# Kernel optimization log

Measured on AMD Instinct MI355X. Metric: run time of the kernel, lower is better.

## Reference

```python
import jax, jax.numpy as jnp
import numpy as np

DIM = 256
HEADS = 8
DIM_HEAD = 64
INNER = HEADS * DIM_HEAD  # 512
SCALE = DIM_HEAD ** -0.5
EPS = 1e-5


def _layernorm(x, w, b):
    mu = jnp.mean(x, axis=-1, keepdims=True)
    var = jnp.var(x, axis=-1, keepdims=True)
    return (x - mu) * jax.lax.rsqrt(var + EPS) * w + b


def setup_inputs() -> dict:
    key = jax.random.key(0)
    ks = jax.random.split(key, 20)
    B, N, M, H, W = 8, 4096, 256, 64, 64
    s = 0.02
    inp = {
        "feat": jax.random.normal(ks[0], (B, N, DIM), jnp.float32),
        "center": jax.random.normal(ks[1], (B, M, DIM), jnp.float32),
        "pos": jax.random.normal(ks[2], (B, DIM, H, W), jnp.float32),
        "center_pos": jax.random.normal(ks[3], (B, M, DIM), jnp.float32),
        # projection weights stored [in, out] so y = x @ W
        "Wq": jax.random.normal(ks[4], (DIM, INNER), jnp.float32) * s,
        "Wk": jax.random.normal(ks[5], (DIM, INNER), jnp.float32) * s,
        "Wv1": jax.random.normal(ks[6], (DIM, INNER), jnp.float32) * s,
        "Wv2": jax.random.normal(ks[7], (DIM, INNER), jnp.float32) * s,
        "Wo1": jax.random.normal(ks[8], (INNER, DIM), jnp.float32) * s,
        "Wo2": jax.random.normal(ks[9], (INNER, DIM), jnp.float32) * s,
        "ln1_w": jnp.ones((DIM,), jnp.float32),
        "ln1_b": jnp.zeros((DIM,), jnp.float32),
        "ln2_w": jnp.ones((DIM,), jnp.float32),
        "ln2_b": jnp.zeros((DIM,), jnp.float32),
        "ffn1_W1": jax.random.normal(ks[10], (DIM, DIM), jnp.float32) * s,
        "ffn1_W2": jax.random.normal(ks[11], (DIM, DIM), jnp.float32) * s,
        "ffn1_b2": jnp.zeros((DIM,), jnp.float32),
        "ffn2_W1": jax.random.normal(ks[12], (DIM, DIM), jnp.float32) * s,
        "ffn2_W2": jax.random.normal(ks[13], (DIM, DIM), jnp.float32) * s,
        "ffn2_b2": jnp.zeros((DIM,), jnp.float32),
    }
    return inp


def reference(feat, center, pos, center_pos, Wq, Wk, Wv1, Wv2, Wo1, Wo2,
              ln1_w, ln1_b, ln2_w, ln2_b, ffn1_W1, ffn1_W2, ffn1_b2,
              ffn2_W1, ffn2_W2, ffn2_b2):
    B = feat.shape[0]
    # pos: [B, C, H, W] -> [B, N, C]
    pos_f = pos.reshape(B, DIM, -1).transpose(0, 2, 1)
    q = (feat + pos_f) @ Wq            # [B, N, INNER]
    k = (center + center_pos) @ Wk     # [B, M, INNER]
    v1 = feat @ Wv1                    # [B, N, INNER]
    v2 = center @ Wv2                  # [B, M, INNER]

    def split(x):  # [B, T, h*d] -> [B, h, T, d]
        return x.reshape(B, x.shape[1], HEADS, DIM_HEAD).transpose(0, 2, 1, 3)

    q, k, v1, v2 = split(q), split(k), split(v1), split(v2)
    attn = jnp.einsum("bhnd,bhmd->bhnm", q, k) * SCALE  # [B, h, N, M]
    attn1 = jax.nn.softmax(attn, axis=-2)  # over N (queries)
    attn2 = jax.nn.softmax(attn, axis=-1)  # over M (keys)
    out_feat = jnp.einsum("bhnm,bhmd->bhnd", attn2, v2)    # [B, h, N, d]
    out_center = jnp.einsum("bhnm,bhnd->bhmd", attn1, v1)  # [B, h, M, d]

    def merge(x):  # [B, h, T, d] -> [B, T, h*d]
        return x.transpose(0, 2, 1, 3).reshape(B, x.shape[2], INNER)

    out_feat = merge(out_feat) @ Wo1 + feat
    out_center = merge(out_center) @ Wo2 + center
    out_feat = _layernorm(out_feat, ln1_w, ln1_b)
    out_center = _layernorm(out_center, ln2_w, ln2_b)
    out_feat = jax.nn.relu(out_feat @ ffn1_W1) @ ffn1_W2 + ffn1_b2 + out_feat
    out_center = jax.nn.relu(out_center @ ffn2_W1) @ ffn2_W2 + ffn2_b2 + out_center
    return out_feat, out_center
```

## Files before the change

kernel.cpp:

```cpp
#include <hip/hip_runtime.h>

typedef __bf16 bf16;
typedef __bf16 bf16x4 __attribute__((ext_vector_type(4)));
typedef __bf16 bf16x8 __attribute__((ext_vector_type(8)));
typedef float f32x4 __attribute__((ext_vector_type(4)));

#define MFMA16(a, b, c) __builtin_amdgcn_mfma_f32_16x16x32_bf16(a, b, c, 0, 0, 0)

#define CEXP 0.18033688011112042f

struct WTArgs {
  const float* src[10];
  bf16* dst[10];
  int K[10];
  int N[10];
};

__global__ __launch_bounds__(256) void wtrans_kernel(WTArgs args) {
  const int z = blockIdx.z;
  const int K = args.K[z], N = args.N[z];
  const int k0 = blockIdx.x * 64, n0 = blockIdx.y * 64;
  if (k0 >= K || n0 >= N) return;
  __shared__ float t[64][65];
  const int tx = threadIdx.x & 63, ty = threadIdx.x >> 6;
  const float* __restrict__ src = args.src[z];
  bf16* __restrict__ dst = args.dst[z];
#pragma unroll
  for (int i = 0; i < 16; ++i)
    t[ty + i * 4][tx] = src[(size_t)(k0 + ty + i * 4) * N + n0 + tx];
  __syncthreads();
#pragma unroll
  for (int i = 0; i < 16; ++i)
    dst[(size_t)(n0 + ty + i * 4) * K + k0 + tx] = (bf16)t[tx][ty + i * 4];
}

__global__ __launch_bounds__(256) void prep_xq_kernel(
    const float* __restrict__ feat, const float* __restrict__ pos,
    bf16* __restrict__ xq) {
  const int n0 = blockIdx.x * 64;
  const int c0 = blockIdx.y * 64;
  const int b = blockIdx.z;
  __shared__ float t[64][65];
  const int tx = threadIdx.x & 63, ty = threadIdx.x >> 6;
#pragma unroll
  for (int i = 0; i < 16; ++i) {
    int c = ty + i * 4;
    t[c][tx] = pos[((size_t)b * 256 + c0 + c) * 4096 + n0 + tx];
  }
  __syncthreads();
#pragma unroll
  for (int i = 0; i < 16; ++i) {
    int n = ty + i * 4;
    size_t off = ((size_t)b * 4096 + n0 + n) * 256 + c0 + tx;
    xq[off] = (bf16)(feat[off] + t[tx][n]);
  }
}

__global__ __launch_bounds__(256) void addvec_kernel(
    const float* __restrict__ a, const float* __restrict__ b,
    bf16* __restrict__ o, int n4) {
  int i = blockIdx.x * 256 + threadIdx.x;
  if (i < n4) {
    f32x4 x = ((const f32x4*)a)[i];
    f32x4 y = ((const f32x4*)b)[i];
    bf16x4 z;
#pragma unroll
    for (int j = 0; j < 4; ++j) z[j] = (bf16)(x[j] + y[j]);
    ((bf16x4*)o)[i] = z;
  }
}

__device__ inline void stage16(const bf16* g, bf16* l) {
  __builtin_amdgcn_global_load_lds(
      (const __attribute__((address_space(1))) void*)g,
      (__attribute__((address_space(3))) void*)l, 16, 0, 0);
}
__device__ inline void stage16(const float* g, bf16* l) {
  f32x4 u = *(const f32x4*)g;
  f32x4 v = *((const f32x4*)g + 1);
  bf16x8 o;
#pragma unroll
  for (int i = 0; i < 4; ++i) {
    o[i] = (bf16)u[i];
    o[4 + i] = (bf16)v[i];
  }
  *(bf16x8*)l = o;
}

template <int EPI, typename TO, typename TR, typename TA>
__global__ __launch_bounds__(256) void gemm_kernel(
    const TA* __restrict__ A, const bf16* __restrict__ BT,
    TO* __restrict__ C, const TR* __restrict__ resid,
    const float* __restrict__ bias, int M, int N, int K) {
  const int m0 = blockIdx.x * 128;
  const int n0 = blockIdx.y * 128;
  const int tid = threadIdx.x;
  const int lane = tid & 63;
  const int w = tid >> 6;
  const int wr = (w >> 1) * 64, wc = (w & 1) * 64;
  const int l15 = lane & 15, quad = lane >> 4;

  __shared__ __align__(16) bf16 Al[128 * 32];
  __shared__ __align__(16) bf16 Bl[128 * 32];

  f32x4 acc[4][4];
#pragma unroll
  for (int i = 0; i < 4; ++i)
#pragma unroll
    for (int j = 0; j < 4; ++j) acc[i][j] = (f32x4){0.f, 0.f, 0.f, 0.f};

  const int sw = (((l15 >> 1) & 3) ^ quad) * 8;

  for (int k0 = 0; k0 < K; k0 += 32) {
#pragma unroll
    for (int c = 0; c < 2; ++c) {
      int idx = tid + c * 256;
      int row = idx >> 2;
      int gs = ((idx & 3) ^ ((row >> 1) & 3)) * 8;
      stage16(A + (size_t)(m0 + row) * K + k0 + gs, Al + idx * 8);
      stage16(BT + (size_t)(n0 + row) * K + k0 + gs, Bl + idx * 8);
    }
    __syncthreads();
    bf16x8 fa[4], fb[4];
#pragma unroll
    for (int i = 0; i < 4; ++i) {
      fa[i] = *(const bf16x8*)(Al + (wr + i * 16 + l15) * 32 + sw);
      fb[i] = *(const bf16x8*)(Bl + (wc + i * 16 + l15) * 32 + sw);
    }
#pragma unroll
    for (int i = 0; i < 4; ++i)
#pragma unroll
      for (int j = 0; j < 4; ++j)
        acc[i][j] = MFMA16(fa[i], fb[j], acc[i][j]);
    __syncthreads();
  }

#pragma unroll
  for (int i = 0; i < 4; ++i) {
#pragma unroll
    for (int r = 0; r < 4; ++r) {
      int row = m0 + wr + i * 16 + quad * 4 + r;
      size_t rb = (size_t)row * N + n0 + wc;
#pragma unroll
      for (int j = 0; j < 4; ++j) {
        int col = j * 16 + l15;
        float v = acc[i][j][r];
        if constexpr (EPI == 1) v = fmaxf(v, 0.f);
        if constexpr (EPI == 2) v += (float)resid[rb + col];
        if constexpr (EPI == 3)
          v += bias[n0 + wc + col] + (float)resid[rb + col];
        C[rb + col] = (TO)v;
      }
    }
  }
}

__global__ __launch_bounds__(256, 1) void attf_kernel(
    const bf16* q, const bf16* __restrict__ kk, const bf16* __restrict__ v1,
    const bf16* __restrict__ v2, bf16* af, float* __restrict__ acc_p,
    float* __restrict__ colsum_p) {
  const int nb = blockIdx.x;
  const int h = blockIdx.y;
  const int b = blockIdx.z;
  const int tid = threadIdx.x;
  const int lane = tid & 63;
  const int w = tid >> 6;
  const int l15 = lane & 15, quad = lane >> 4;

  __shared__ __align__(16) bf16 klds[256 * 72];
  __shared__ __align__(16) bf16 v2T[64 * 264];
  __shared__ __align__(16) bf16 v1T[2][64 * 72];
  __shared__ __align__(16) bf16 PT[256 * 72];
  __shared__ __align__(16) bf16 Pl[4][16 * 264];

#pragma unroll
  for (int c = 0; c < 8; ++c) {
    int idx = tid + c * 256;
    int m = idx >> 3;
    int dc = (idx & 7) * 8;
    *(bf16x8*)(klds + m * 72 + dc) =
        *(const bf16x8*)(kk + ((size_t)(b * 256 + m)) * 512 + h * 64 + dc);
  }
#pragma unroll
  for (int c = 0; c < 8; ++c) {
    int idx = tid + c * 256;
    int m = idx >> 3;
    int dc = (idx & 7) * 8;
    bf16x8 t =
        *(const bf16x8*)(v2 + ((size_t)(b * 256 + m)) * 512 + h * 64 + dc);
#pragma unroll
    for (int j = 0; j < 8; ++j) v2T[(dc + j) * 264 + m] = t[j];
  }
  {
    const int nl = tid >> 3;
    const int dc = (tid & 7) * 8;
    const bf16* v1b =
        v1 + ((size_t)(b * 4096 + nb * 1024)) * 512 + h * 64 + dc;
    bf16x8 t0 = *(const bf16x8*)(v1b + (size_t)nl * 512);
    bf16x8 t1 = *(const bf16x8*)(v1b + (size_t)(nl + 32) * 512);
#pragma unroll
    for (int j = 0; j < 8; ++j) {
      v1T[0][(dc + j) * 72 + nl] = t0[j];
      v1T[0][(dc + j) * 72 + nl + 32] = t1[j];
    }
  }
  bf16x8 qa0, qa1;
  {
    int nrow = b * 4096 + nb * 1024 + w * 16 + l15;
    const bf16* qp = q + (size_t)nrow * 512 + h * 64 + quad * 8;
    qa0 = *(const bf16x8*)(qp);
    qa1 = *(const bf16x8*)(qp + 32);
  }

  f32x4 oc2[16];
#pragma unroll
  for (int i = 0; i < 16; ++i) oc2[i] = (f32x4){0.f, 0.f, 0.f, 0.f};
  float cs[16];
#pragma unroll
  for (int i = 0; i < 16; ++i) cs[i] = 0.f;

  __syncthreads();

#pragma unroll 2
  for (int ch = 0; ch < 16; ++ch) {
    bf16x8 v1a, v1b;
    const int nl = tid >> 3;
    const int dc = (tid & 7) * 8;
    if (ch < 15) {
      const bf16* v1p =
          v1 + ((size_t)(b * 4096 + nb * 1024 + (ch + 1) * 64)) * 512 +
          h * 64 + dc;
      v1a = *(const bf16x8*)(v1p + (size_t)nl * 512);
      v1b = *(const bf16x8*)(v1p + (size_t)(nl + 32) * 512);
    }

    float rs[4] = {0.f, 0.f, 0.f, 0.f};
#pragma unroll
    for (int mt = 0; mt < 16; ++mt) {
      const bf16* kp = klds + (mt * 16 + l15) * 72 + quad * 8;
      bf16x8 b0 = *(const bf16x8*)(kp);
      bf16x8 b1 = *(const bf16x8*)(kp + 32);
      f32x4 s = (f32x4){0.f, 0.f, 0.f, 0.f};
      s = MFMA16(qa0, b0, s);
      s = MFMA16(qa1, b1, s);
      float e0 = exp2f(s[0] * CEXP);
      float e1 = exp2f(s[1] * CEXP);
      float e2 = exp2f(s[2] * CEXP);
      float e3 = exp2f(s[3] * CEXP);
      rs[0] += e0; rs[1] += e1; rs[2] += e2; rs[3] += e3;
      cs[mt] += e0 + e1 + e2 + e3;
      Pl[w][(quad * 4 + 0) * 264 + mt * 16 + l15] = (bf16)e0;
      Pl[w][(quad * 4 + 1) * 264 + mt * 16 + l15] = (bf16)e1;
      Pl[w][(quad * 4 + 2) * 264 + mt * 16 + l15] = (bf16)e2;
      Pl[w][(quad * 4 + 3) * 264 + mt * 16 + l15] = (bf16)e3;
      bf16x4 ev;
      ev[0] = (bf16)e0; ev[1] = (bf16)e1; ev[2] = (bf16)e2; ev[3] = (bf16)e3;
      *(bf16x4*)(PT + (mt * 16 + l15) * 72 + w * 16 + quad * 4) = ev;
    }
    if (ch < 15) {
      bf16* dst = v1T[(ch + 1) & 1];
#pragma unroll
      for (int j = 0; j < 8; ++j) {
        dst[(dc + j) * 72 + nl] = v1a[j];
        dst[(dc + j) * 72 + nl + 32] = v1b[j];
      }
    }
    __syncthreads();

    bf16x8 qn0 = qa0, qn1 = qa1;
    if (ch < 15) {
      int nrow = b * 4096 + nb * 1024 + (ch + 1) * 64 + w * 16 + l15;
      const bf16* qp = q + (size_t)nrow * 512 + h * 64 + quad * 8;
      qn0 = *(const bf16x8*)(qp);
      qn1 = *(const bf16x8*)(qp + 32);
    }

    f32x4 o1[4];
#pragma unroll
    for (int i = 0; i < 4; ++i) o1[i] = (f32x4){0.f, 0.f, 0.f, 0.f};
#pragma unroll
    for (int ks = 0; ks < 8; ++ks) {
      bf16x8 pa = *(const bf16x8*)(Pl[w] + l15 * 264 + ks * 32 + quad * 8);
#pragma unroll
      for (int dt = 0; dt < 4; ++dt) {
        bf16x8 vb = *(const bf16x8*)(v2T + (dt * 16 + l15) * 264 + ks * 32 +
                                     quad * 8);
        o1[dt] = MFMA16(pa, vb, o1[dt]);
      }
    }
    float inv[4];
#pragma unroll
    for (int r = 0; r < 4; ++r) {
      float v = rs[r];
      v += __shfl_xor(v, 1, 64);
      v += __shfl_xor(v, 2, 64);
      v += __shfl_xor(v, 4, 64);
      v += __shfl_xor(v, 8, 64);
      inv[r] = 1.f / v;
    }
#pragma unroll
    for (int dt = 0; dt < 4; ++dt) {
#pragma unroll
      for (int r = 0; r < 4; ++r) {
        int n = nb * 1024 + ch * 64 + w * 16 + quad * 4 + r;
        af[((size_t)(b * 4096 + n)) * 512 + h * 64 + dt * 16 + l15] =
            (bf16)(o1[dt][r] * inv[r]);
      }
    }

    const bf16* vc = v1T[ch & 1];
#pragma unroll
    for (int ks = 0; ks < 2; ++ks) {
      bf16x8 vbv[4];
#pragma unroll
      for (int dt = 0; dt < 4; ++dt)
        vbv[dt] = *(const bf16x8*)(vc + (dt * 16 + l15) * 72 + ks * 32 +
                                   quad * 8);
#pragma unroll
      for (int mq = 0; mq < 4; ++mq) {
        bf16x8 pa2 = *(const bf16x8*)(PT + (mq * 64 + w * 16 + l15) * 72 +
                                      ks * 32 + quad * 8);
#pragma unroll
        for (int dt = 0; dt < 4; ++dt)
          oc2[mq * 4 + dt] = MFMA16(pa2, vbv[dt], oc2[mq * 4 + dt]);
      }
    }
    __syncthreads();
    qa0 = qn0;
    qa1 = qn1;
  }

  float* cw = (float*)klds;
#pragma unroll
  for (int t = 0; t < 16; ++t) {
    float v = cs[t];
    v += __shfl_xor(v, 16, 64);
    v += __shfl_xor(v, 32, 64);
    if (quad == 0) cw[w * 256 + t * 16 + l15] = v;
  }
  __syncthreads();
  {
    int m = tid;
    float s = cw[m] + cw[256 + m] + cw[512 + m] + cw[768 + m];
    colsum_p[((size_t)(nb * 64 + b * 8 + h)) * 256 + m] = s;
  }
  float* base = acc_p + ((size_t)(nb * 64 + b * 8 + h)) * 256 * 64;
#pragma unroll
  for (int mq = 0; mq < 4; ++mq) {
#pragma unroll
    for (int dt = 0; dt < 4; ++dt) {
#pragma unroll
      for (int r = 0; r < 4; ++r) {
        int m = mq * 64 + w * 16 + quad * 4 + r;
        base[m * 64 + dt * 16 + l15] = oc2[mq * 4 + dt][r];
      }
    }
  }
}

__global__ __launch_bounds__(256) void acm_kernel(
    const float* __restrict__ acc_p, const float* __restrict__ colsum_p,
    bf16* __restrict__ acm) {
  int idx = blockIdx.x * 256 + threadIdx.x;
  int d = idx & 63;
  int h = (idx >> 6) & 7;
  int m = (idx >> 9) & 255;
  int b = idx >> 17;
  float cv = 0.f, v = 0.f;
#pragma unroll
  for (int p = 0; p < 4; ++p) {
    cv += colsum_p[((size_t)(p * 64 + b * 8 + h)) * 256 + m];
    v += acc_p[(((size_t)(p * 64 + b * 8 + h)) * 256 + m) * 64 + d];
  }
  acm[idx] = (bf16)(v / cv);
}

__global__ __launch_bounds__(256) void ln_kernel(
    const bf16* __restrict__ x, const float* __restrict__ wv,
    const float* __restrict__ bv, bf16* __restrict__ y, int rows) {
  int wave = threadIdx.x >> 6;
  int lane = threadIdx.x & 63;
  int row = blockIdx.x * 4 + wave;
  if (row >= rows) return;
  const bf16* xr = x + (size_t)row * 256;
  bf16x4 v = *(const bf16x4*)(xr + lane * 4);
  float f0 = v[0], f1 = v[1], f2 = v[2], f3 = v[3];
  float s = f0 + f1 + f2 + f3;
  float ss = f0 * f0 + f1 * f1 + f2 * f2 + f3 * f3;
#pragma unroll
  for (int m = 1; m < 64; m <<= 1) {
    s += __shfl_xor(s, m, 64);
    ss += __shfl_xor(ss, m, 64);
  }
  float mean = s * (1.f / 256.f);
  float var = ss * (1.f / 256.f) - mean * mean;
  float rstd = rsqrtf(var + 1e-5f);
  f32x4 wq = *(const f32x4*)(wv + lane * 4);
  f32x4 bq = *(const f32x4*)(bv + lane * 4);
  bf16x4 o;
  o[0] = (bf16)((f0 - mean) * rstd * wq[0] + bq[0]);
  o[1] = (bf16)((f1 - mean) * rstd * wq[1] + bq[1]);
  o[2] = (bf16)((f2 - mean) * rstd * wq[2] + bq[2]);
  o[3] = (bf16)((f3 - mean) * rstd * wq[3] + bq[3]);
  *(bf16x4*)(y + (size_t)row * 256 + lane * 4) = o;
}

extern "C" void kernel_launch(void* const* d_in, const int* in_sizes, int n_in,
                              void* d_out, int out_size, void* d_ws,
                              size_t ws_size, hipStream_t stream) {
  const float* feat = (const float*)d_in[0];
  const float* center = (const float*)d_in[1];
  const float* pos = (const float*)d_in[2];
  const float* cpos = (const float*)d_in[3];
  const float* Wq = (const float*)d_in[4];
  const float* Wk = (const float*)d_in[5];
  const float* Wv1 = (const float*)d_in[6];
  const float* Wv2 = (const float*)d_in[7];
  const float* Wo1 = (const float*)d_in[8];
  const float* Wo2 = (const float*)d_in[9];
  const float* ln1w = (const float*)d_in[10];
  const float* ln1b = (const float*)d_in[11];
  const float* ln2w = (const float*)d_in[12];
  const float* ln2b = (const float*)d_in[13];
  const float* f1W1 = (const float*)d_in[14];
  const float* f1W2 = (const float*)d_in[15];
  const float* f1b2 = (const float*)d_in[16];
  const float* f2W1 = (const float*)d_in[17];
  const float* f2W2 = (const float*)d_in[18];
  const float* f2b2 = (const float*)d_in[19];

  char* ws = (char*)d_ws;
  const size_t MB = 1024 * 1024;
  bf16* q_ = (bf16*)(ws + 0);
  bf16* af_ = q_;
  bf16* v1_ = (bf16*)(ws + 32 * MB);
  bf16* xq_ = (bf16*)(ws + 64 * MB);
  float* accp_ = (float*)(ws + 64 * MB);
  bf16* rf_ = xq_;
  bf16* k_ = (bf16*)(ws + 80 * MB);
  bf16* xk_ = (bf16*)(ws + 82 * MB);
  bf16* rc_ = xk_;
  bf16* v2_ = (bf16*)(ws + 83 * MB);
  bf16* acm_ = v2_;
  float* colsum_ = (float*)(ws + 89 * MB);
  bf16* wt_ = (bf16*)(ws + 89 * MB + 262144);
  bf16* yf_ = q_;
  bf16* tf_ = (bf16*)(ws + 16 * MB);
  bf16* yc_ = (bf16*)(ws + 92 * MB);
  bf16* tc_ = (bf16*)(ws + 93 * MB);

  bf16* WqT = wt_;
  bf16* WkT = WqT + 131072;
  bf16* Wv1T = WkT + 131072;
  bf16* Wv2T = Wv1T + 131072;
  bf16* Wo1T = Wv2T + 131072;
  bf16* Wo2T = Wo1T + 131072;
  bf16* f1W1T = Wo2T + 131072;
  bf16* f1W2T = f1W1T + 65536;
  bf16* f2W1T = f1W2T + 65536;
  bf16* f2W2T = f2W1T + 65536;

  float* out_feat = (float*)d_out;
  float* out_center = out_feat + (size_t)8 * 4096 * 256;

  WTArgs wa;
  const float* srcs[10] = {Wq, Wk, Wv1, Wv2, Wo1, Wo2, f1W1, f1W2, f2W1, f2W2};
  bf16* dsts[10] = {WqT, WkT, Wv1T, Wv2T, Wo1T, Wo2T, f1W1T, f1W2T, f2W1T, f2W2T};
  int Ks[10] = {256, 256, 256, 256, 512, 512, 256, 256, 256, 256};
  int Ns[10] = {512, 512, 512, 512, 256, 256, 256, 256, 256, 256};
  for (int i = 0; i < 10; ++i) {
    wa.src[i] = srcs[i];
    wa.dst[i] = dsts[i];
    wa.K[i] = Ks[i];
    wa.N[i] = Ns[i];
  }

  wtrans_kernel<<<dim3(8, 8, 10), 256, 0, stream>>>(wa);
  prep_xq_kernel<<<dim3(64, 4, 8), 256, 0, stream>>>(feat, pos, xq_);
  addvec_kernel<<<dim3(512), 256, 0, stream>>>(center, cpos, xk_, 131072);

  gemm_kernel<0, bf16, bf16, bf16><<<dim3(256, 4), 256, 0, stream>>>(
      xq_, WqT, q_, nullptr, nullptr, 32768, 512, 256);
  gemm_kernel<0, bf16, bf16, bf16><<<dim3(16, 4), 256, 0, stream>>>(
      xk_, WkT, k_, nullptr, nullptr, 2048, 512, 256);
  gemm_kernel<0, bf16, bf16, float><<<dim3(256, 4), 256, 0, stream>>>(
      feat, Wv1T, v1_, nullptr, nullptr, 32768, 512, 256);
  gemm_kernel<0, bf16, bf16, float><<<dim3(16, 4), 256, 0, stream>>>(
      center, Wv2T, v2_, nullptr, nullptr, 2048, 512, 256);

  attf_kernel<<<dim3(4, 8, 8), 256, 0, stream>>>(q_, k_, v1_, v2_, af_, accp_,
                                                 colsum_);
  acm_kernel<<<dim3(4096), 256, 0, stream>>>(accp_, colsum_, acm_);

  gemm_kernel<2, bf16, float, bf16><<<dim3(256, 2), 256, 0, stream>>>(
      af_, Wo1T, rf_, feat, nullptr, 32768, 256, 512);
  ln_kernel<<<dim3(8192), 256, 0, stream>>>(rf_, ln1w, ln1b, yf_, 32768);
  gemm_kernel<1, bf16, bf16, bf16><<<dim3(256, 2), 256, 0, stream>>>(
      yf_, f1W1T, tf_, nullptr, nullptr, 32768, 256, 256);
  gemm_kernel<3, float, bf16, bf16><<<dim3(256, 2), 256, 0, stream>>>(
      tf_, f1W2T, out_feat, yf_, f1b2, 32768, 256, 256);

  gemm_kernel<2, bf16, float, bf16><<<dim3(16, 2), 256, 0, stream>>>(
      acm_, Wo2T, rc_, center, nullptr, 2048, 256, 512);
  ln_kernel<<<dim3(512), 256, 0, stream>>>(rc_, ln2w, ln2b, yc_, 2048);
  gemm_kernel<1, bf16, bf16, bf16><<<dim3(16, 2), 256, 0, stream>>>(
      yc_, f2W1T, tc_, nullptr, nullptr, 2048, 256, 256);
  gemm_kernel<3, float, bf16, bf16><<<dim3(16, 2), 256, 0, stream>>>(
      tc_, f2W2T, out_center, yc_, f2b2, 2048, 256, 256);
}
```

Before: 387.3 us.

## Batch feat/center GEMMs, fuse center add into K GEMM, vectorize epilogues

The center+center_pos add is folded into the K-projection GEMM's A staging, and paired feat/center GEMMs and layernorms now run as single launches using a blockIdx.z selector. MFMA operand order is swapped so each lane holds four consecutive columns. This lets the GEMM and attention epilogues write vectorized bf16x4/f32x4 stores instead of scattered scalar ones. The aim is fewer launches, less small-launch tail time, and better store coalescing. The cost is that the z=1 center launches spawn many blocks that return immediately.

```diff
diff --git a/kernel.cpp b/kernel.cpp
--- a/kernel.cpp
+++ b/kernel.cpp
@@ -56,20 +56,6 @@
   }
 }
 
-__global__ __launch_bounds__(256) void addvec_kernel(
-    const float* __restrict__ a, const float* __restrict__ b,
-    bf16* __restrict__ o, int n4) {
-  int i = blockIdx.x * 256 + threadIdx.x;
-  if (i < n4) {
-    f32x4 x = ((const f32x4*)a)[i];
-    f32x4 y = ((const f32x4*)b)[i];
-    bf16x4 z;
-#pragma unroll
-    for (int j = 0; j < 4; ++j) z[j] = (bf16)(x[j] + y[j]);
-    ((bf16x4*)o)[i] = z;
-  }
-}
-
 __device__ inline void stage16(const bf16* g, bf16* l) {
   __builtin_amdgcn_global_load_lds(
       (const __attribute__((address_space(1))) void*)g,
@@ -86,13 +72,52 @@
   }
   *(bf16x8*)l = o;
 }
-
-template <int EPI, typename TO, typename TR, typename TA>
-__global__ __launch_bounds__(256) void gemm_kernel(
-    const TA* __restrict__ A, const bf16* __restrict__ BT,
-    TO* __restrict__ C, const TR* __restrict__ resid,
-    const float* __restrict__ bias, int M, int N, int K) {
+__device__ inline void stage16(const float* g, const float* g2, bf16* l) {
+  f32x4 u = *(const f32x4*)g + *(const f32x4*)g2;
+  f32x4 v = *((const f32x4*)g + 1) + *((const f32x4*)g2 + 1);
+  bf16x8 o;
+#pragma unroll
+  for (int i = 0; i < 4; ++i) {
+    o[i] = (bf16)u[i];
+    o[4 + i] = (bf16)v[i];
+  }
+  *(bf16x8*)l = o;
+}
+
+__device__ inline f32x4 rload(const float* p) { return *(const f32x4*)p; }
+__device__ inline f32x4 rload(const bf16* p) {
+  bf16x4 t = *(const bf16x4*)p;
+  return (f32x4){(float)t[0], (float)t[1], (float)t[2], (float)t[3]};
+}
+__device__ inline void cstore(float* p, f32x4 v) { *(f32x4*)p = v; }
+__device__ inline void cstore(bf16* p, f32x4 v) {
+  bf16x4 o;
+  o[0] = (bf16)v[0]; o[1] = (bf16)v[1]; o[2] = (bf16)v[2]; o[3] = (bf16)v[3];
+  *(bf16x4*)p = o;
+}
+
+struct GArg {
+  const void* A[2];
+  const void* A2[2];
+  const bf16* BT[2];
+  void* C[2];
+  const void* resid[2];
+  const float* bias[2];
+  int M[2];
+};
+
+template <int EPI, typename TO, typename TR, typename TA, bool FUSE2>
+__global__ __launch_bounds__(256) void gemm_kernel(GArg g, int N, int K) {
+  const int z = blockIdx.z;
   const int m0 = blockIdx.x * 128;
+  if (m0 >= g.M[z]) return;
+  const TA* A = (const TA*)g.A[z];
+  const TA* A2 = (const TA*)g.A2[z];
+  const bf16* BT = g.BT[z];
+  TO* C = (TO*)g.C[z];
+  const TR* resid = (const TR*)g.resid[z];
+  const float* bias = g.bias[z];
+
   const int n0 = blockIdx.y * 128;
   const int tid = threadIdx.x;
   const int lane = tid & 63;
@@ -117,7 +142,11 @@
       int idx = tid + c * 256;
       int row = idx >> 2;
       int gs = ((idx & 3) ^ ((row >> 1) & 3)) * 8;
-      stage16(A + (size_t)(m0 + row) * K + k0 + gs, Al + idx * 8);
+      size_t aoff = (size_t)(m0 + row) * K + k0 + gs;
+      if constexpr (FUSE2)
+        stage16(A + aoff, A2 + aoff, Al + idx * 8);
+      else
+        stage16(A + aoff, Al + idx * 8);
       stage16(BT + (size_t)(n0 + row) * K + k0 + gs, Bl + idx * 8);
     }
     __syncthreads();
@@ -131,26 +160,26 @@
     for (int i = 0; i < 4; ++i)
 #pragma unroll
       for (int j = 0; j < 4; ++j)
-        acc[i][j] = MFMA16(fa[i], fb[j], acc[i][j]);
+        acc[i][j] = MFMA16(fb[j], fa[i], acc[i][j]);
     __syncthreads();
   }
 
 #pragma unroll
   for (int i = 0; i < 4; ++i) {
 #pragma unroll
-    for (int r = 0; r < 4; ++r) {
-      int row = m0 + wr + i * 16 + quad * 4 + r;
-      size_t rb = (size_t)row * N + n0 + wc;
-#pragma unroll
-      for (int j = 0; j < 4; ++j) {
-        int col = j * 16 + l15;
-        float v = acc[i][j][r];
-        if constexpr (EPI == 1) v = fmaxf(v, 0.f);
-        if constexpr (EPI == 2) v += (float)resid[rb + col];
-        if constexpr (EPI == 3)
-          v += bias[n0 + wc + col] + (float)resid[rb + col];
-        C[rb + col] = (TO)v;
+    for (int j = 0; j < 4; ++j) {
+      int row = m0 + wr + i * 16 + l15;
+      int col = n0 + wc + j * 16 + quad * 4;
+      size_t off = (size_t)row * N + col;
+      f32x4 v = acc[i][j];
+      if constexpr (EPI == 1) {
+#pragma unroll
+        for (int e = 0; e < 4; ++e) v[e] = fmaxf(v[e], 0.f);
       }
+      if constexpr (EPI == 2) v += rload(resid + off);
+      if constexpr (EPI == 3)
+        v += rload(resid + off) + *(const f32x4*)(bias + col);
+      cstore(C + off, v);
     }
   }
 }
@@ -285,10 +314,9 @@
       for (int dt = 0; dt < 4; ++dt) {
         bf16x8 vb = *(const bf16x8*)(v2T + (dt * 16 + l15) * 264 + ks * 32 +
                                      quad * 8);
-        o1[dt] = MFMA16(pa, vb, o1[dt]);
+        o1[dt] = MFMA16(vb, pa, o1[dt]);
       }
     }
-    float inv[4];
 #pragma unroll
     for (int r = 0; r < 4; ++r) {
       float v = rs[r];
@@ -296,15 +324,27 @@
       v += __shfl_xor(v, 2, 64);
       v += __shfl_xor(v, 4, 64);
       v += __shfl_xor(v, 8, 64);
-      inv[r] = 1.f / v;
-    }
-#pragma unroll
-    for (int dt = 0; dt < 4; ++dt) {
-#pragma unroll
-      for (int r = 0; r < 4; ++r) {
-        int n = nb * 1024 + ch * 64 + w * 16 + quad * 4 + r;
-        af[((size_t)(b * 4096 + n)) * 512 + h * 64 + dt * 16 + l15] =
-            (bf16)(o1[dt][r] * inv[r]);
+      rs[r] = v;
+    }
+    {
+      int srcq = (l15 >> 2) << 4;
+      float s0 = __shfl(rs[0], srcq, 64);
+      float s1 = __shfl(rs[1], srcq, 64);
+      float s2 = __shfl(rs[2], srcq, 64);
+      float s3 = __shfl(rs[3], srcq, 64);
+      float a01 = (l15 & 1) ? s1 : s0;
+      float a23 = (l15 & 1) ? s3 : s2;
+      float inv = 1.f / ((l15 & 2) ? a23 : a01);
+      int n = nb * 1024 + ch * 64 + w * 16 + l15;
+      bf16* ap = af + ((size_t)(b * 4096 + n)) * 512 + h * 64 + quad * 4;
+#pragma unroll
+      for (int dt = 0; dt < 4; ++dt) {
+        bf16x4 ov;
+        ov[0] = (bf16)(o1[dt][0] * inv);
+        ov[1] = (bf16)(o1[dt][1] * inv);
+        ov[2] = (bf16)(o1[dt][2] * inv);
+        ov[3] = (bf16)(o1[dt][3] * inv);
+        *(bf16x4*)(ap + dt * 16) = ov;
       }
     }
 
@@ -322,7 +362,7 @@
                                       ks * 32 + quad * 8);
 #pragma unroll
         for (int dt = 0; dt < 4; ++dt)
-          oc2[mq * 4 + dt] = MFMA16(pa2, vbv[dt], oc2[mq * 4 + dt]);
+          oc2[mq * 4 + dt] = MFMA16(vbv[dt], pa2, oc2[mq * 4 + dt]);
       }
     }
     __syncthreads();
@@ -347,14 +387,10 @@
   float* base = acc_p + ((size_t)(nb * 64 + b * 8 + h)) * 256 * 64;
 #pragma unroll
   for (int mq = 0; mq < 4; ++mq) {
-#pragma unroll
-    for (int dt = 0; dt < 4; ++dt) {
-#pragma unroll
-      for (int r = 0; r < 4; ++r) {
-        int m = mq * 64 + w * 16 + quad * 4 + r;
-        base[m * 64 + dt * 16 + l15] = oc2[mq * 4 + dt][r];
-      }
-    }
+    int m = mq * 64 + w * 16 + l15;
+#pragma unroll
+    for (int dt = 0; dt < 4; ++dt)
+      *(f32x4*)(base + m * 64 + dt * 16 + quad * 4) = oc2[mq * 4 + dt];
   }
 }
 
@@ -376,12 +412,23 @@
 }
 
 __global__ __launch_bounds__(256) void ln_kernel(
-    const bf16* __restrict__ x, const float* __restrict__ wv,
-    const float* __restrict__ bv, bf16* __restrict__ y, int rows) {
+    const bf16* __restrict__ x0, const bf16* __restrict__ x1,
+    const float* __restrict__ w0, const float* __restrict__ b0,
+    const float* __restrict__ w1, const float* __restrict__ b1,
+    bf16* __restrict__ y0, bf16* __restrict__ y1, int rows0, int rows1) {
   int wave = threadIdx.x >> 6;
   int lane = threadIdx.x & 63;
   int row = blockIdx.x * 4 + wave;
-  if (row >= rows) return;
+  const bf16* x;
+  const float *wv, *bv;
+  bf16* y;
+  if (row < rows0) {
+    x = x0; wv = w0; bv = b0; y = y0;
+  } else {
+    row -= rows0;
+    if (row >= rows1) return;
+    x = x1; wv = w1; bv = b1; y = y1;
+  }
   const bf16* xr = x + (size_t)row * 256;
   bf16x4 v = *(const bf16x4*)(xr + lane * 4);
   float f0 = v[0], f1 = v[1], f2 = v[2], f3 = v[3];
@@ -438,8 +485,7 @@
   float* accp_ = (float*)(ws + 64 * MB);
   bf16* rf_ = xq_;
   bf16* k_ = (bf16*)(ws + 80 * MB);
-  bf16* xk_ = (bf16*)(ws + 82 * MB);
-  bf16* rc_ = xk_;
+  bf16* rc_ = (bf16*)(ws + 82 * MB);
   bf16* v2_ = (bf16*)(ws + 83 * MB);
   bf16* acm_ = v2_;
   float* colsum_ = (float*)(ws + 89 * MB);
@@ -477,34 +523,64 @@
 
   wtrans_kernel<<<dim3(8, 8, 10), 256, 0, stream>>>(wa);
   prep_xq_kernel<<<dim3(64, 4, 8), 256, 0, stream>>>(feat, pos, xq_);
-  addvec_kernel<<<dim3(512), 256, 0, stream>>>(center, cpos, xk_, 131072);
-
-  gemm_kernel<0, bf16, bf16, bf16><<<dim3(256, 4), 256, 0, stream>>>(
-      xq_, WqT, q_, nullptr, nullptr, 32768, 512, 256);
-  gemm_kernel<0, bf16, bf16, bf16><<<dim3(16, 4), 256, 0, stream>>>(
-      xk_, WkT, k_, nullptr, nullptr, 2048, 512, 256);
-  gemm_kernel<0, bf16, bf16, float><<<dim3(256, 4), 256, 0, stream>>>(
-      feat, Wv1T, v1_, nullptr, nullptr, 32768, 512, 256);
-  gemm_kernel<0, bf16, bf16, float><<<dim3(16, 4), 256, 0, stream>>>(
-      center, Wv2T, v2_, nullptr, nullptr, 2048, 512, 256);
+
+  {
+    GArg a{};
+    a.A[0] = xq_; a.BT[0] = WqT; a.C[0] = q_; a.M[0] = 32768;
+    gemm_kernel<0, bf16, bf16, bf16, false>
+        <<<dim3(256, 4, 1), 256, 0, stream>>>(a, 512, 256);
+  }
+  {
+    GArg a{};
+    a.A[0] = center; a.A2[0] = cpos; a.BT[0] = WkT; a.C[0] = k_;
+    a.M[0] = 2048;
+    gemm_kernel<0, bf16, bf16, float, true>
+        <<<dim3(16, 4, 1), 256, 0, stream>>>(a, 512, 256);
+  }
+  {
+    GArg a{};
+    a.A[0] = feat; a.A[1] = center;
+    a.BT[0] = Wv1T; a.BT[1] = Wv2T;
+    a.C[0] = v1_; a.C[1] = v2_;
+    a.M[0] = 32768; a.M[1] = 2048;
+    gemm_kernel<0, bf16, bf16, float, false>
+        <<<dim3(256, 4, 2), 256, 0, stream>>>(a, 512, 256);
+  }
 
   attf_kernel<<<dim3(4, 8, 8), 256, 0, stream>>>(q_, k_, v1_, v2_, af_, accp_,
                                                  colsum_);
   acm_kernel<<<dim3(4096), 256, 0, stream>>>(accp_, colsum_, acm_);
 
-  gemm_kernel<2, bf16, float, bf16><<<dim3(256, 2), 256, 0, stream>>>(
-      af_, Wo1T, rf_, feat, nullptr, 32768, 256, 512);
-  ln_kernel<<<dim3(8192), 256, 0, stream>>>(rf_, ln1w, ln1b, yf_, 32768);
-  gemm_kernel<1, bf16, bf16, bf16><<<dim3(256, 2), 256, 0, stream>>>(
-      yf_, f1W1T, tf_, nullptr, nullptr, 32768, 256, 256);
-  gemm_kernel<3, float, bf16, bf16><<<dim3(256, 2), 256, 0, stream>>>(
-      tf_, f1W2T, out_feat, yf_, f1b2, 32768, 256, 256);
-
-  gemm_kernel<2, bf16, float, bf16><<<dim3(16, 2), 256, 0, stream>>>(
-      acm_, Wo2T, rc_, center, nullptr, 2048, 256, 512);
-  ln_kernel<<<dim3(512), 256, 0, stream>>>(rc_, ln2w, ln2b, yc_, 2048);
-  gemm_kernel<1, bf16, bf16, bf16><<<dim3(16, 2), 256, 0, stream>>>(
-      yc_, f2W1T, tc_, nullptr, nullptr, 2048, 256, 256);
-  gemm_kernel<3, float, bf16, bf16><<<dim3(16, 2), 256, 0, stream>>>(
-      tc_, f2W2T, out_center, yc_, f2b2, 2048, 256, 256);
-}
+  {
+    GArg a{};
+    a.A[0] = af_; a.A[1] = acm_;
+    a.BT[0] = Wo1T; a.BT[1] = Wo2T;
+    a.C[0] = rf_; a.C[1] = rc_;
+    a.resid[0] = feat; a.resid[1] = center;
+    a.M[0] = 32768; a.M[1] = 2048;
+    gemm_kernel<2, bf16, float, bf16, false>
+        <<<dim3(256, 2, 2), 256, 0, stream>>>(a, 256, 512);
+  }
+  ln_kernel<<<dim3(8704), 256, 0, stream>>>(rf_, rc_, ln1w, ln1b, ln2w, ln2b,
+                                            yf_, yc_, 32768, 2048);
+  {
+    GArg a{};
+    a.A[0] = yf_; a.A[1] = yc_;
+    a.BT[0] = f1W1T; a.BT[1] = f2W1T;
+    a.C[0] = tf_; a.C[1] = tc_;
+    a.M[0] = 32768; a.M[1] = 2048;
+    gemm_kernel<1, bf16, bf16, bf16, false>
+        <<<dim3(256, 2, 2), 256, 0, stream>>>(a, 256, 256);
+  }
+  {
+    GArg a{};
+    a.A[0] = tf_; a.A[1] = tc_;
+    a.BT[0] = f1W2T; a.BT[1] = f2W2T;
+    a.C[0] = out_feat; a.C[1] = out_center;
+    a.resid[0] = yf_; a.resid[1] = yc_;
+    a.bias[0] = f1b2; a.bias[1] = f2b2;
+    a.M[0] = 32768; a.M[1] = 2048;
+    gemm_kernel<3, float, bf16, bf16, false>
+        <<<dim3(256, 2, 2), 256, 0, stream>>>(a, 256, 256);
+  }
+}
```

New measurement: 379.6 us. -2.0%, faster.
